# Optimization experiments

Measured on AMD Instinct MI355X. Metric: run time of the kernel, lower is better.

Reference implementation:

```python
import jax, jax.numpy as jnp
import numpy as np

# ---- module hyperparameters (init_kwargs) ----
M = 6          # truncation level
D = 5          # path dimension
C = 4.0        # phi parameter
A = 1.0        # phi parameter a
SIGLEN = (D ** (M + 1) - 1) // (D - 1) - 1  # 19530
B, S = 64, 32  # batch x samples
N_BISECT = 100

# level id (1..M) of each signature coordinate: d^k coords at level k
LEVELS = jnp.asarray(np.repeat(np.arange(1, M + 1), [D ** k for k in range(1, M + 1)]), dtype=jnp.float32)  # [L]
# one-hot [L, M] mapping coordinates to their level, for per-level squared-norm sums
LEVEL_ONEHOT = jnp.asarray((np.repeat(np.arange(1, M + 1), [D ** k for k in range(1, M + 1)])[:, None] == np.arange(1, M + 1)[None, :]).astype(np.float32))


def setup_inputs() -> dict:
    key = jax.random.key(0)
    signatures = jax.random.normal(key, (B, S, SIGLEN), dtype=jnp.float32) * 0.5
    return {"signatures": signatures}


def _phi(x):
    # phi(x) = x for x <= C, else C + C^(1+a) (C^-a - x^-a)/a
    return jnp.where(x > C, C + C ** (1.0 + A) * (C ** (-A) - x ** (-A)) / A, x)


def _dilatation_norm(x):
    """x: [B,S,L] signatures. Returns norm lambda in [0,1], shape [B,S,1].
    Solves c0 + sum_k c_k t^{2k} = 0 on [0,2] by bisection (replaces brentq)."""
    x2 = x * x
    norm_quad = 1.0 + jnp.sum(x2, axis=-1)          # [B,S]
    c0 = 1.0 - _phi(norm_quad)                      # [B,S], <= 0
    ck = jnp.einsum('bsl,lm->bsm', x2, LEVEL_ONEHOT)  # [B,S,M] per-level squared norms
    coeffs = jnp.concatenate([c0[..., None], ck], axis=-1)  # [B,S,M+1]
    ks = jnp.arange(M + 1, dtype=jnp.float32)

    def poly(t):  # t: [B,S]
        return jnp.sum(coeffs * (t[..., None] ** 2) ** ks, axis=-1)

    def body(i, carry):
        lo, hi = carry
        mid = 0.5 * (lo + hi)
        neg = poly(mid) < 0.0
        return jnp.where(neg, mid, lo), jnp.where(neg, hi, mid)

    lo = jnp.zeros_like(c0)
    hi = jnp.full_like(c0, 2.0)
    lo, hi = jax.lax.fori_loop(0, N_BISECT, body, (lo, hi))
    root = 0.5 * (lo + hi)
    root = jnp.where(jnp.all(jnp.isfinite(coeffs), axis=-1), root, 0.0)
    root = jnp.minimum(root, 1.0)  # clamp as in dilatation()
    return root[..., None]          # [B,S,1]


def reference(signatures):
    # Normalization.apply + rescale + mean over samples (martingale_indices=None path)
    norm = _dilatation_norm(signatures)                       # [B,S,1]
    scaled = signatures * norm ** LEVELS[None, None, :]       # [B,S,L]
    return jnp.mean(scaled, axis=-2)                          # [B,L]
```

## Files before the change

kernel.cpp:

```cpp
#include <hip/hip_runtime.h>
#include <math.h>

#define BATCH   64
#define SAMP    32
#define SIGLEN  19530
#define NROWS   (BATCH * SAMP)
#define NF2     (SIGLEN / 2)
#define NF4     4882
#define NBISECT 40


__device__ __forceinline__ int level0(int l) {
    return (l >= 5) + (l >= 30) + (l >= 155) + (l >= 780) + (l >= 3905);
}

__device__ __forceinline__ float sumsq_region(const float* __restrict__ row,
                                              int lo, int hi, int par, int t) {
    float acc = 0.f;
    int vstart = lo + ((par - lo) % 4 + 4) % 4;
    if (vstart > hi) vstart = hi;
    const int nvec = (hi - vstart) >> 2;
    for (int l = lo + t; l < vstart; l += 256) { float v = row[l]; acc += v * v; }
    const float4* __restrict__ p = (const float4*)(row + vstart);
    for (int j = t; j < nvec; j += 256) {
        float4 v = p[j];
        acc += v.x * v.x + v.y * v.y + v.z * v.z + v.w * v.w;
    }
    for (int l = vstart + 4 * nvec + t; l < hi; l += 256) { float v = row[l]; acc += v * v; }
    return acc;
}

__global__ __launch_bounds__(256) void sums_bisect_kernel(
        const float* __restrict__ x, float* __restrict__ pw) {
    const int bs = blockIdx.x;
    const float* __restrict__ row = x + (size_t)bs * SIGLEN;
    const int t = threadIdx.x;
    const int par = (bs & 1) * 2;

    float a1 = sumsq_region(row,    0,     5, par, t);
    float a2 = sumsq_region(row,    5,    30, par, t);
    float a3 = sumsq_region(row,   30,   155, par, t);
    float a4 = sumsq_region(row,  155,   780, par, t);
    float a5 = sumsq_region(row,  780,  3905, par, t);
    float a6 = sumsq_region(row, 3905, SIGLEN, par, t);

    #pragma unroll
    for (int off = 32; off > 0; off >>= 1) {
        a1 += __shfl_xor(a1, off);
        a2 += __shfl_xor(a2, off);
        a3 += __shfl_xor(a3, off);
        a4 += __shfl_xor(a4, off);
        a5 += __shfl_xor(a5, off);
        a6 += __shfl_xor(a6, off);
    }

    __shared__ float red[4][6];
    const int wave = t >> 6, lane = t & 63;
    if (lane == 0) {
        red[wave][0] = a1; red[wave][1] = a2; red[wave][2] = a3;
        red[wave][3] = a4; red[wave][4] = a5; red[wave][5] = a6;
    }
    __syncthreads();

    if (t == 0) {
        float s1 = 0.f, s2 = 0.f, s3 = 0.f, s4 = 0.f, s5 = 0.f, s6 = 0.f;
        #pragma unroll
        for (int w = 0; w < 4; ++w) {
            s1 += red[w][0]; s2 += red[w][1]; s3 += red[w][2];
            s4 += red[w][3]; s5 += red[w][4]; s6 += red[w][5];
        }
        const float total = s1 + s2 + s3 + s4 + s5 + s6;
        const float nq = 1.0f + total;
        const float phi = (nq > 4.0f) ? (8.0f - 16.0f / nq) : nq;
        const float c0 = 1.0f - phi;
        const bool fin = isfinite(c0) && isfinite(total);

        float lo = 0.0f, hi = 2.0f;
        #pragma unroll 4
        for (int i = 0; i < NBISECT; ++i) {
            const float mid = 0.5f * (lo + hi);
            const float u = mid * mid;
            const float p = ((((((s6 * u + s5) * u + s4) * u + s3) * u + s2) * u + s1) * u) + c0;
            const bool neg = p < 0.0f;
            lo = neg ? mid : lo;
            hi = neg ? hi : mid;
        }
        float root = 0.5f * (lo + hi);
        if (!fin) root = 0.0f;
        root = fminf(root, 1.0f);

        float* dst = pw + (size_t)bs * 6;
        const float inv = 1.0f / SAMP;
        float w1 = root;
        float w2 = w1 * root, w3 = w2 * root, w4 = w3 * root, w5 = w4 * root, w6 = w5 * root;
        dst[0] = w1 * inv; dst[1] = w2 * inv; dst[2] = w3 * inv;
        dst[3] = w4 * inv; dst[4] = w5 * inv; dst[5] = w6 * inv;
    }
}

__global__ __launch_bounds__(256) void scale_mean_kernel(
        const float* __restrict__ x, const float* __restrict__ pw,
        float* __restrict__ out) {
    const int b = blockIdx.y;
    const int t = threadIdx.x;

    __shared__ float w[SAMP * 6];
    if (t < SAMP * 6) w[t] = pw[(size_t)b * (SAMP * 6) + t];
    __syncthreads();

    const int q = blockIdx.x * 256 + t;
    if (q > NF4) return;
    const bool full = (q < NF4);

    const int e0 = 4 * q;
    const int levA = level0(e0);
    const int levZ = full ? level0(e0 + 3) : level0(e0 + 1);

    const float2* __restrict__ xp =
        (const float2*)x + (size_t)b * (SAMP * NF2) + 2 * q;

    float acc0 = 0.f, acc1 = 0.f, acc2 = 0.f, acc3 = 0.f;
    if (levA == levZ) {
        #pragma unroll 8
        for (int s = 0; s < SAMP; ++s) {
            const float ws = w[s * 6 + levA];
            const float2 v0 = xp[(size_t)s * NF2];
            acc0 += v0.x * ws; acc1 += v0.y * ws;
            if (full) {
                const float2 v1 = xp[(size_t)s * NF2 + 1];
                acc2 += v1.x * ws; acc3 += v1.y * ws;
            }
        }
    } else {
        const int l0 = level0(e0), l1 = level0(e0 + 1);
        const int l2 = level0(e0 + 2), l3 = level0(e0 + 3);
        #pragma unroll 8
        for (int s = 0; s < SAMP; ++s) {
            const float2 v0 = xp[(size_t)s * NF2];
            acc0 += v0.x * w[s * 6 + l0]; acc1 += v0.y * w[s * 6 + l1];
            if (full) {
                const float2 v1 = xp[(size_t)s * NF2 + 1];
                acc2 += v1.x * w[s * 6 + l2]; acc3 += v1.y * w[s * 6 + l3];
            }
        }
    }

    float2* __restrict__ op = (float2*)out + (size_t)b * NF2 + 2 * q;
    float2 r0; r0.x = acc0; r0.y = acc1;
    op[0] = r0;
    if (full) { float2 r1; r1.x = acc2; r1.y = acc3; op[1] = r1; }
}

extern "C" void kernel_launch(void* const* d_in, const int* in_sizes, int n_in,
                              void* d_out, int out_size, void* d_ws, size_t ws_size,
                              hipStream_t stream) {
    const float* x = (const float*)d_in[0];
    float* out = (float*)d_out;
    float* pw = (float*)d_ws;

    sums_bisect_kernel<<<NROWS, 256, 0, stream>>>(x, pw);

    dim3 gridB((NF4 + 1 + 255) / 256, BATCH);
    scale_mean_kernel<<<gridB, 256, 0, stream>>>(x, pw, out);
}
```

Before: 258.3 us.

## Fuse norm-bisection and scaled-mean kernels into one cooperative kernel with grid sync

Merges the per-row sum/bisection kernel and the scale-and-mean kernel into a single cooperative launch of 1024 blocks. Each block first handles two rows, then a grid-wide sync, then a 611-element chunk of one batch's output. The aim is to drop the second launch and keep the input resident in the large cache between phases. The cost is a grid barrier, fewer blocks per phase, and narrower float2 loads with less parallelism in the second phase.

```diff
diff --git a/kernel.cpp b/kernel.cpp
--- a/kernel.cpp
+++ b/kernel.cpp
@@ -1,14 +1,18 @@
 #include <hip/hip_runtime.h>
+#include <hip/hip_cooperative_groups.h>
 #include <math.h>
+
+namespace cg = cooperative_groups;
 
 #define BATCH   64
 #define SAMP    32
 #define SIGLEN  19530
 #define NROWS   (BATCH * SAMP)
 #define NF2     (SIGLEN / 2)
-#define NF4     4882
 #define NBISECT 40
-
+#define NBLK    1024
+#define CHUNKS_PER_B 16
+#define CHUNK   611
 
 __device__ __forceinline__ int level0(int l) {
     return (l >= 5) + (l >= 30) + (l >= 155) + (l >= 780) + (l >= 3905);
@@ -30,125 +34,114 @@
     return acc;
 }
 
-__global__ __launch_bounds__(256) void sums_bisect_kernel(
-        const float* __restrict__ x, float* __restrict__ pw) {
-    const int bs = blockIdx.x;
-    const float* __restrict__ row = x + (size_t)bs * SIGLEN;
+__global__ __launch_bounds__(256, 4) void fused_kernel(
+        const float* __restrict__ x, float* __restrict__ pw,
+        float* __restrict__ out) {
     const int t = threadIdx.x;
-    const int par = (bs & 1) * 2;
+    __shared__ float red[4][6];
+    __shared__ float w[SAMP * 6];
 
-    float a1 = sumsq_region(row,    0,     5, par, t);
-    float a2 = sumsq_region(row,    5,    30, par, t);
-    float a3 = sumsq_region(row,   30,   155, par, t);
-    float a4 = sumsq_region(row,  155,   780, par, t);
-    float a5 = sumsq_region(row,  780,  3905, par, t);
-    float a6 = sumsq_region(row, 3905, SIGLEN, par, t);
+    #pragma unroll 1
+    for (int r = 0; r < 2; ++r) {
+        const int rowi = 2 * blockIdx.x + r;
+        const float* __restrict__ row = x + (size_t)rowi * SIGLEN;
+        const int par = (rowi & 1) * 2;
 
-    #pragma unroll
-    for (int off = 32; off > 0; off >>= 1) {
-        a1 += __shfl_xor(a1, off);
-        a2 += __shfl_xor(a2, off);
-        a3 += __shfl_xor(a3, off);
-        a4 += __shfl_xor(a4, off);
-        a5 += __shfl_xor(a5, off);
-        a6 += __shfl_xor(a6, off);
+        float a1 = sumsq_region(row,    0,     5, par, t);
+        float a2 = sumsq_region(row,    5,    30, par, t);
+        float a3 = sumsq_region(row,   30,   155, par, t);
+        float a4 = sumsq_region(row,  155,   780, par, t);
+        float a5 = sumsq_region(row,  780,  3905, par, t);
+        float a6 = sumsq_region(row, 3905, SIGLEN, par, t);
+
+        #pragma unroll
+        for (int off = 32; off > 0; off >>= 1) {
+            a1 += __shfl_xor(a1, off);
+            a2 += __shfl_xor(a2, off);
+            a3 += __shfl_xor(a3, off);
+            a4 += __shfl_xor(a4, off);
+            a5 += __shfl_xor(a5, off);
+            a6 += __shfl_xor(a6, off);
+        }
+        const int wave = t >> 6, lane = t & 63;
+        if (lane == 0) {
+            red[wave][0] = a1; red[wave][1] = a2; red[wave][2] = a3;
+            red[wave][3] = a4; red[wave][4] = a5; red[wave][5] = a6;
+        }
+        __syncthreads();
+
+        if (t == 0) {
+            float s1 = 0.f, s2 = 0.f, s3 = 0.f, s4 = 0.f, s5 = 0.f, s6 = 0.f;
+            #pragma unroll
+            for (int wv = 0; wv < 4; ++wv) {
+                s1 += red[wv][0]; s2 += red[wv][1]; s3 += red[wv][2];
+                s4 += red[wv][3]; s5 += red[wv][4]; s6 += red[wv][5];
+            }
+            const float total = s1 + s2 + s3 + s4 + s5 + s6;
+            const float nq = 1.0f + total;
+            const float phi = (nq > 4.0f) ? (8.0f - 16.0f / nq) : nq;
+            const float c0 = 1.0f - phi;
+            const bool fin = isfinite(c0) && isfinite(total);
+
+            float lo = 0.0f, hi = 2.0f;
+            #pragma unroll 4
+            for (int i = 0; i < NBISECT; ++i) {
+                const float mid = 0.5f * (lo + hi);
+                const float u = mid * mid;
+                const float p = ((((((s6 * u + s5) * u + s4) * u + s3) * u + s2) * u + s1) * u) + c0;
+                const bool neg = p < 0.0f;
+                lo = neg ? mid : lo;
+                hi = neg ? hi : mid;
+            }
+            float root = 0.5f * (lo + hi);
+            if (!fin) root = 0.0f;
+            root = fminf(root, 1.0f);
+
+            float* dst = pw + (size_t)rowi * 6;
+            const float inv = 1.0f / SAMP;
+            float w1 = root;
+            float w2 = w1 * root, w3 = w2 * root, w4 = w3 * root, w5 = w4 * root, w6 = w5 * root;
+            dst[0] = w1 * inv; dst[1] = w2 * inv; dst[2] = w3 * inv;
+            dst[3] = w4 * inv; dst[4] = w5 * inv; dst[5] = w6 * inv;
+        }
+        __syncthreads();
     }
 
-    __shared__ float red[4][6];
-    const int wave = t >> 6, lane = t & 63;
-    if (lane == 0) {
-        red[wave][0] = a1; red[wave][1] = a2; red[wave][2] = a3;
-        red[wave][3] = a4; red[wave][4] = a5; red[wave][5] = a6;
-    }
-    __syncthreads();
+    cg::this_grid().sync();
 
-    if (t == 0) {
-        float s1 = 0.f, s2 = 0.f, s3 = 0.f, s4 = 0.f, s5 = 0.f, s6 = 0.f;
-        #pragma unroll
-        for (int w = 0; w < 4; ++w) {
-            s1 += red[w][0]; s2 += red[w][1]; s3 += red[w][2];
-            s4 += red[w][3]; s5 += red[w][4]; s6 += red[w][5];
-        }
-        const float total = s1 + s2 + s3 + s4 + s5 + s6;
-        const float nq = 1.0f + total;
-        const float phi = (nq > 4.0f) ? (8.0f - 16.0f / nq) : nq;
-        const float c0 = 1.0f - phi;
-        const bool fin = isfinite(c0) && isfinite(total);
-
-        float lo = 0.0f, hi = 2.0f;
-        #pragma unroll 4
-        for (int i = 0; i < NBISECT; ++i) {
-            const float mid = 0.5f * (lo + hi);
-            const float u = mid * mid;
-            const float p = ((((((s6 * u + s5) * u + s4) * u + s3) * u + s2) * u + s1) * u) + c0;
-            const bool neg = p < 0.0f;
-            lo = neg ? mid : lo;
-            hi = neg ? hi : mid;
-        }
-        float root = 0.5f * (lo + hi);
-        if (!fin) root = 0.0f;
-        root = fminf(root, 1.0f);
-
-        float* dst = pw + (size_t)bs * 6;
-        const float inv = 1.0f / SAMP;
-        float w1 = root;
-        float w2 = w1 * root, w3 = w2 * root, w4 = w3 * root, w5 = w4 * root, w6 = w5 * root;
-        dst[0] = w1 * inv; dst[1] = w2 * inv; dst[2] = w3 * inv;
-        dst[3] = w4 * inv; dst[4] = w5 * inv; dst[5] = w6 * inv;
-    }
-}
-
-__global__ __launch_bounds__(256) void scale_mean_kernel(
-        const float* __restrict__ x, const float* __restrict__ pw,
-        float* __restrict__ out) {
-    const int b = blockIdx.y;
-    const int t = threadIdx.x;
-
-    __shared__ float w[SAMP * 6];
+    const int b = blockIdx.x / CHUNKS_PER_B;
+    const int c = blockIdx.x % CHUNKS_PER_B;
     if (t < SAMP * 6) w[t] = pw[(size_t)b * (SAMP * 6) + t];
     __syncthreads();
 
-    const int q = blockIdx.x * 256 + t;
-    if (q > NF4) return;
-    const bool full = (q < NF4);
+    const int j0 = c * CHUNK;
+    int jend = j0 + CHUNK; if (jend > NF2) jend = NF2;
 
-    const int e0 = 4 * q;
-    const int levA = level0(e0);
-    const int levZ = full ? level0(e0 + 3) : level0(e0 + 1);
+    const float2* __restrict__ xp = (const float2*)x + (size_t)b * (SAMP * NF2);
+    float2* __restrict__ op = (float2*)out + (size_t)b * NF2;
 
-    const float2* __restrict__ xp =
-        (const float2*)x + (size_t)b * (SAMP * NF2) + 2 * q;
-
-    float acc0 = 0.f, acc1 = 0.f, acc2 = 0.f, acc3 = 0.f;
-    if (levA == levZ) {
-        #pragma unroll 8
-        for (int s = 0; s < SAMP; ++s) {
-            const float ws = w[s * 6 + levA];
-            const float2 v0 = xp[(size_t)s * NF2];
-            acc0 += v0.x * ws; acc1 += v0.y * ws;
-            if (full) {
-                const float2 v1 = xp[(size_t)s * NF2 + 1];
-                acc2 += v1.x * ws; acc3 += v1.y * ws;
+    for (int j = j0 + t; j < jend; j += 256) {
+        const int l0 = level0(2 * j);
+        const int l1 = level0(2 * j + 1);
+        float acc0 = 0.f, acc1 = 0.f;
+        if (l0 == l1) {
+            #pragma unroll 8
+            for (int s = 0; s < SAMP; ++s) {
+                const float ws = w[s * 6 + l0];
+                const float2 v = xp[(size_t)s * NF2 + j];
+                acc0 += v.x * ws; acc1 += v.y * ws;
+            }
+        } else {
+            #pragma unroll 8
+            for (int s = 0; s < SAMP; ++s) {
+                const float2 v = xp[(size_t)s * NF2 + j];
+                acc0 += v.x * w[s * 6 + l0];
+                acc1 += v.y * w[s * 6 + l1];
             }
         }
-    } else {
-        const int l0 = level0(e0), l1 = level0(e0 + 1);
-        const int l2 = level0(e0 + 2), l3 = level0(e0 + 3);
-        #pragma unroll 8
-        for (int s = 0; s < SAMP; ++s) {
-            const float2 v0 = xp[(size_t)s * NF2];
-            acc0 += v0.x * w[s * 6 + l0]; acc1 += v0.y * w[s * 6 + l1];
-            if (full) {
-                const float2 v1 = xp[(size_t)s * NF2 + 1];
-                acc2 += v1.x * w[s * 6 + l2]; acc3 += v1.y * w[s * 6 + l3];
-            }
-        }
+        float2 r; r.x = acc0; r.y = acc1;
+        op[j] = r;
     }
-
-    float2* __restrict__ op = (float2*)out + (size_t)b * NF2 + 2 * q;
-    float2 r0; r0.x = acc0; r0.y = acc1;
-    op[0] = r0;
-    if (full) { float2 r1; r1.x = acc2; r1.y = acc3; op[1] = r1; }
 }
 
 extern "C" void kernel_launch(void* const* d_in, const int* in_sizes, int n_in,
@@ -158,8 +151,7 @@
     float* out = (float*)d_out;
     float* pw = (float*)d_ws;
 
-    sums_bisect_kernel<<<NROWS, 256, 0, stream>>>(x, pw);
-
-    dim3 gridB((NF4 + 1 + 255) / 256, BATCH);
-    scale_mean_kernel<<<gridB, 256, 0, stream>>>(x, pw, out);
+    void* args[] = { (void*)&x, (void*)&pw, (void*)&out };
+    hipLaunchCooperativeKernel((const void*)fused_kernel,
+                               dim3(NBLK), dim3(256), args, 0, stream);
 }
```

After: 369.1 us. 42.9% more time.
